# Kernel tuning notes

Measured on AMD Instinct MI355X. Metric: run time of the kernel, lower is better.

Reference implementation:

```python
import jax, jax.numpy as jnp
import numpy as np

N = 100000
K = 16
E = N * K
IN_DIM = 16
MLP_DIMS = (32, 32, 16)


def setup_inputs() -> dict:
    key = jax.random.key(0)
    ks = jax.random.split(key, 10)
    feats = jax.random.normal(ks[0], (N, IN_DIM), dtype=jnp.float32)
    xyz = jax.random.normal(ks[1], (N, 3), dtype=jnp.float32)
    neighbors_index = jax.random.randint(ks[2], (E,), 0, N, dtype=jnp.int32)
    neighbors_row_splits = (jnp.arange(N + 1, dtype=jnp.int32) * K)
    neighbors_distance = jax.random.uniform(ks[3], (E,), dtype=jnp.float32)
    # MLP params: 4 -> 32 (relu) -> 32 (relu) -> IN_DIM * MLP_DIMS[-1]
    def dense(k, fan_in, fan_out):
        lim = np.sqrt(6.0 / (fan_in + fan_out)).astype(np.float32)
        W = jax.random.uniform(k, (fan_in, fan_out), minval=-lim, maxval=lim, dtype=jnp.float32)
        b = jnp.zeros((fan_out,), dtype=jnp.float32)
        return W, b
    W1, b1 = dense(ks[4], 4, MLP_DIMS[0])
    W2, b2 = dense(ks[5], MLP_DIMS[0], MLP_DIMS[1])
    W3, b3 = dense(ks[6], MLP_DIMS[1], IN_DIM * MLP_DIMS[2])
    return {"feats": feats, "xyz": xyz, "neighbors_index": neighbors_index,
            "neighbors_row_splits": neighbors_row_splits,
            "neighbors_distance": neighbors_distance,
            "W1": W1, "b1": b1, "W2": W2, "b2": b2, "W3": W3, "b3": b3}


def reference(feats, xyz, neighbors_index, neighbors_row_splits, neighbors_distance,
              W1, b1, W2, b2, W3, b3):
    n_queries = neighbors_row_splits.shape[0] - 1
    counts = neighbors_row_splits[1:] - neighbors_row_splits[:-1]
    # ragged row_splits -> per-edge segment ids (query index per edge)
    segment_ids = jnp.repeat(jnp.arange(n_queries, dtype=jnp.int32), counts,
                             total_repeat_length=neighbors_index.shape[0])
    # gather neighbor coords, subtract query coords
    diff = xyz[neighbors_index] - xyz[segment_ids]          # [E, 3]
    d = jax.lax.stop_gradient(neighbors_distance)
    r = jnp.sqrt(d + 1e-7)                                   # [E]
    polar = jnp.stack([r, diff[:, 0] / r, diff[:, 2] / r, diff[:, 1] / r], axis=-1)  # [E, 4]
    # per-edge MLP producing dynamic weight matrices
    h = jax.nn.relu(polar @ W1 + b1)
    h = jax.nn.relu(h @ W2 + b2)
    w = (h @ W3 + b3).reshape(-1, IN_DIM, MLP_DIMS[2])       # [E, in_dim, out]
    neighbor_feats = feats[neighbors_index]                  # [E, in_dim]
    edge_out = jnp.einsum('ei,eio->eo', neighbor_feats, w)   # [E, out]
    new_feats = jax.ops.segment_sum(edge_out, segment_ids, num_segments=n_queries)
    return new_feats
```

## Files before the change

### kernel.cpp

```cpp
#include <hip/hip_runtime.h>


constexpr int THREADS = 256;
constexpr int NBLOCKS = 1024;

typedef __attribute__((ext_vector_type(8)))  short short8;
typedef __attribute__((ext_vector_type(4)))  int   intx4;
typedef __attribute__((ext_vector_type(16))) float floatx16;
typedef __attribute__((ext_vector_type(2)))  float floatx2;

static __device__ inline short f2bf(float x) {
  __bf16 b = (__bf16)x;
  return __builtin_bit_cast(short, b);
}
static __device__ inline unsigned pk2(float lo, float hi) {
  unsigned l = (unsigned short)__builtin_bit_cast(unsigned short, f2bf(lo));
  unsigned h = (unsigned short)__builtin_bit_cast(unsigned short, f2bf(hi));
  return (h << 16) | l;
}

template <int CTRL>
static __device__ inline float dpp_add(float x) {
  int y = __builtin_amdgcn_update_dpp(0, __builtin_bit_cast(int, x),
                                      CTRL, 0xF, 0xF, true);
  return x + __builtin_bit_cast(float, y);
}

__global__ __launch_bounds__(THREADS, 2) void polarconv_v14(
    const float* __restrict__ feats,
    const float* __restrict__ xyz,
    const int*   __restrict__ nbr,
    const float* __restrict__ dist,
    const float* __restrict__ W1,
    const float* __restrict__ b1,
    const float* __restrict__ W2,
    const float* __restrict__ b2,
    const float* __restrict__ W3,
    const float* __restrict__ b3,
    float* __restrict__ out,
    int Nq)
{
  const int tid  = threadIdx.x;
  const int lane = tid & 63;
  const int col  = lane & 31;
  const int g2   = lane >> 5;
  const int qh   = col >> 4;
  const int c16  = col & 15;
  const int E    = Nq * 16;

  __shared__ alignas(16) short sBU[1024 * 8];
  short8* sBU8 = reinterpret_cast<short8*>(sBU);
  for (int s = tid; s < 1024; s += THREADS) {
    const int t2h = s >> 6, ln = s & 63;
    const int t2 = t2h >> 1, h = t2h & 1;
    const int cc = ln & 31, gg = ln >> 5;
    short8 v;
#pragma unroll
    for (int j = 0; j < 8; ++j)
      v[j] = f2bf(W3[(16 * h + (j & 3) + 8 * (j >> 2) + 4 * gg) * 256 + t2 * 32 + cc]);
    sBU8[s] = v;
  }
  __syncthreads();
  const short8* buP = sBU8 + lane;

  short8 a1;
#pragma unroll
  for (int j = 0; j < 8; ++j) {
    short v = 0;
    if (g2 == 0) {
      if (j < 4)       v = f2bf(W1[j * 32 + col]);
      else if (j == 4) v = f2bf(b1[col]);
    }
    a1[j] = v;
  }
  short8 a2k[2];
#pragma unroll
  for (int h = 0; h < 2; ++h)
#pragma unroll
    for (int j = 0; j < 8; ++j)
      a2k[h][j] = f2bf(W2[(16 * h + (j & 3) + 8 * (j >> 2) + 4 * g2) * 32 + col]);
  short8 ab3;
#pragma unroll
  for (int j = 0; j < 8; ++j)
    ab3[j] = (col < 16) ? f2bf(b3[(8 * g2 + j) * 16 + col]) : (short)0;

  floatx16 z16;
#pragma unroll
  for (int m = 0; m < 16; ++m) z16[m] = 0.0f;

  const int wid   = blockIdx.x * (THREADS / 64) + (tid >> 6);
  const int STR   = NBLOCKS * (THREADS / 64);
  const int pairs = (Nq + 1) >> 1;
  int p = wid;
  if (p >= pairs) return;

  int   nbN;
  float dN, cxN, cyN, czN, nxN, nyN, nzN;
  {
    const int e = min(p * 32 + col, E - 1);
    nbN = nbr[e];
    dN  = dist[e];
    const int qc = min(2 * p + qh, Nq - 1);
    cxN = xyz[3 * qc]; cyN = xyz[3 * qc + 1]; czN = xyz[3 * qc + 2];
    nxN = xyz[3 * nbN]; nyN = xyz[3 * nbN + 1]; nzN = xyz[3 * nbN + 2];
  }

  for (; p < pairs; p += STR) {
    const int   nbA = nbN;
    const float dA = dN, cx = cxN, cy = cyN, cz = czN;
    const float nx = nxN, ny = nyN, nz = nzN;

    const float4* fp = reinterpret_cast<const float4*>(feats + (size_t)nbA * 16);
    float4 v0 = fp[0], v1 = fp[1], v2 = fp[2], v3 = fp[3];

    const int pc = min(p + STR, pairs - 1);
    {
      const int e2 = min(pc * 32 + col, E - 1);
      nbN = nbr[e2];
      dN  = dist[e2];
      const int qc2 = min(2 * pc + qh, Nq - 1);
      cxN = xyz[3 * qc2]; cyN = xyz[3 * qc2 + 1]; czN = xyz[3 * qc2 + 2];
    }

    const float rr  = sqrtf(dA + 1e-7f);
    const float inv = 1.0f / rr;
    const float q0 = rr;
    const float q1 = (nx - cx) * inv;
    const float q2 = (nz - cz) * inv;
    const float q3 = (ny - cy) * inv;

    short8 bp;
    bp[0] = (g2 == 0) ? f2bf(q0) : (short)0;
    bp[1] = (g2 == 0) ? f2bf(q1) : (short)0;
    bp[2] = (g2 == 0) ? f2bf(q2) : (short)0;
    bp[3] = (g2 == 0) ? f2bf(q3) : (short)0;
    bp[4] = (g2 == 0) ? (short)0x3F80 : (short)0;
    bp[5] = 0; bp[6] = 0; bp[7] = 0;

    floatx16 d1 = __builtin_amdgcn_mfma_f32_32x32x16_bf16(a1, bp, z16, 0, 0, 0);
    short8 bh1k0, bh1k1;
#pragma unroll
    for (int j = 0; j < 8; ++j) {
      bh1k0[j] = f2bf(fmaxf(d1[j], 0.0f));
      bh1k1[j] = f2bf(fmaxf(d1[8 + j], 0.0f));
    }

    floatx16 t0 = __builtin_amdgcn_mfma_f32_32x32x16_bf16(a2k[0], bh1k0, z16, 0, 0, 0);
    floatx16 d2 = __builtin_amdgcn_mfma_f32_32x32x16_bf16(a2k[1], bh1k1, t0, 0, 0, 0);
    short8 bh2k0, bh2k1;
#pragma unroll
    for (int j = 0; j < 8; ++j) {
      const int c0 = (j & 3) + 8 * (j >> 2);
      const float bl0 = g2 ? b2[c0 + 4]      : b2[c0];
      const float bl1 = g2 ? b2[16 + c0 + 4] : b2[16 + c0];
      bh2k0[j] = f2bf(fmaxf(d2[j]     + bl0, 0.0f));
      bh2k1[j] = f2bf(fmaxf(d2[8 + j] + bl1, 0.0f));
    }

    nxN = xyz[3 * nbN]; nyN = xyz[3 * nbN + 1]; nzN = xyz[3 * nbN + 2];

    unsigned fpk0 = pk2(v0.x, v0.y), fpk1 = pk2(v0.z, v0.w);
    unsigned fpk2 = pk2(v1.x, v1.y), fpk3 = pk2(v1.z, v1.w);
    unsigned fpk4 = pk2(v2.x, v2.y), fpk5 = pk2(v2.z, v2.w);
    unsigned fpk6 = pk2(v3.x, v3.y), fpk7 = pk2(v3.z, v3.w);

    intx4 bsel;
    bsel[0] = (int)(g2 ? fpk4 : fpk0);
    bsel[1] = (int)(g2 ? fpk5 : fpk1);
    bsel[2] = (int)(g2 ? fpk6 : fpk2);
    bsel[3] = (int)(g2 ? fpk7 : fpk3);
    short8 bf3 = __builtin_bit_cast(short8, bsel);
    floatx16 s3 = __builtin_amdgcn_mfma_f32_32x32x16_bf16(ab3, bf3, z16, 0, 0, 0);
    floatx2 Sb[4];
#pragma unroll
    for (int r = 0; r < 4; ++r) { Sb[r][0] = s3[2 * r]; Sb[r][1] = s3[2 * r + 1]; }

#pragma unroll
    for (int t2 = 0; t2 < 8; ++t2) {
      short8 w0 = buP[(t2 * 2 + 0) * 64];
      short8 w1 = buP[(t2 * 2 + 1) * 64];
      floatx16 u0 = __builtin_amdgcn_mfma_f32_32x32x16_bf16(w0, bh2k0, z16, 0, 0, 0);
      floatx16 dd = __builtin_amdgcn_mfma_f32_32x32x16_bf16(w1, bh2k1, u0, 0, 0, 0);
      unsigned fw;
      switch (t2) {
        case 0: fw = fpk0; break; case 1: fw = fpk1; break;
        case 2: fw = fpk2; break; case 3: fw = fpk3; break;
        case 4: fw = fpk4; break; case 5: fw = fpk5; break;
        case 6: fw = fpk6; break; default: fw = fpk7; break;
      }
      const float fe = __builtin_bit_cast(float, (int)(fw << 16));
      const float fo = __builtin_bit_cast(float, (int)(fw & 0xffff0000u));
      const floatx2 fe2 = {fe, fe}, fo2 = {fo, fo};
#pragma unroll
      for (int r = 0; r < 4; ++r) {
        floatx2 lo = {dd[2 * r],     dd[2 * r + 1]};
        floatx2 hi = {dd[8 + 2 * r], dd[8 + 2 * r + 1]};
        Sb[r] = __builtin_elementwise_fma(fe2, lo, Sb[r]);
        Sb[r] = __builtin_elementwise_fma(fo2, hi, Sb[r]);
      }
      if (t2 & 1) __builtin_amdgcn_sched_barrier(0);
    }

    float Sa[8];
#pragma unroll
    for (int r = 0; r < 4; ++r) { Sa[2 * r] = Sb[r][0]; Sa[2 * r + 1] = Sb[r][1]; }

#pragma unroll
    for (int j = 0; j < 8; ++j) Sa[j] = dpp_add<0xB1>(Sa[j]);
#pragma unroll
    for (int j = 0; j < 8; ++j) Sa[j] = dpp_add<0x4E>(Sa[j]);
#pragma unroll
    for (int j = 0; j < 8; ++j) Sa[j] = dpp_add<0x124>(Sa[j]);
#pragma unroll
    for (int j = 0; j < 8; ++j) Sa[j] = dpp_add<0x128>(Sa[j]);

    if (c16 == 0) {
      const int qq = 2 * p + qh;
      if (qq < Nq) {
        float* op = out + (size_t)qq * 16 + 4 * g2;
        float4 lo = {Sa[0], Sa[1], Sa[2], Sa[3]};
        float4 hi = {Sa[4], Sa[5], Sa[6], Sa[7]};
        *reinterpret_cast<float4*>(op)     = lo;
        *reinterpret_cast<float4*>(op + 8) = hi;
      }
    }
  }
}

extern "C" void kernel_launch(void* const* d_in, const int* in_sizes, int n_in,
                              void* d_out, int out_size, void* d_ws, size_t ws_size,
                              hipStream_t stream) {
  const float* feats = (const float*)d_in[0];
  const float* xyz   = (const float*)d_in[1];
  const int*   nbr   = (const int*)d_in[2];
  const float* dist  = (const float*)d_in[4];
  const float* W1 = (const float*)d_in[5];
  const float* b1 = (const float*)d_in[6];
  const float* W2 = (const float*)d_in[7];
  const float* b2 = (const float*)d_in[8];
  const float* W3 = (const float*)d_in[9];
  const float* b3 = (const float*)d_in[10];
  float* out = (float*)d_out;

  const int Nq = in_sizes[3] - 1;

  polarconv_v14<<<NBLOCKS, THREADS, 0, stream>>>(
      feats, xyz, nbr, dist, W1, b1, W2, b2, W3, b3, out, Nq);
}
```

Before: 56.99 us.

## Software-pipeline MLP layers 1-2 of next pair with layer-3 contraction of current pair

Splits the per-pair work into two phases: phase1 computes the first two MLP layers and packs the features, and phase2 runs the W3 MFMA contraction, the reduction and the store. The loop now runs phase1 for the next pair before phase2 for the current one, with index and coordinate loads prefetched two iterations ahead. The aim is to overlap the dependent MFMA chains and memory latency of two pairs. The sched_barrier hints are removed, and carrying a second set of live state raises register pressure, which may cut occupancy or cause spills.

```diff
diff --git a/kernel.cpp b/kernel.cpp
--- a/kernel.cpp
+++ b/kernel.cpp
@@ -26,7 +26,12 @@
   return x + __builtin_bit_cast(float, y);
 }
 
-__global__ __launch_bounds__(THREADS, 2) void polarconv_v14(
+struct P1out {
+  short8 bh0, bh1;
+  unsigned f[8];
+};
+
+__global__ __launch_bounds__(THREADS, 2) void polarconv_v16(
     const float* __restrict__ feats,
     const float* __restrict__ xyz,
     const int*   __restrict__ nbr,
@@ -88,41 +93,11 @@
 #pragma unroll
   for (int m = 0; m < 16; ++m) z16[m] = 0.0f;
 
-  const int wid   = blockIdx.x * (THREADS / 64) + (tid >> 6);
-  const int STR   = NBLOCKS * (THREADS / 64);
-  const int pairs = (Nq + 1) >> 1;
-  int p = wid;
-  if (p >= pairs) return;
-
-  int   nbN;
-  float dN, cxN, cyN, czN, nxN, nyN, nzN;
-  {
-    const int e = min(p * 32 + col, E - 1);
-    nbN = nbr[e];
-    dN  = dist[e];
-    const int qc = min(2 * p + qh, Nq - 1);
-    cxN = xyz[3 * qc]; cyN = xyz[3 * qc + 1]; czN = xyz[3 * qc + 2];
-    nxN = xyz[3 * nbN]; nyN = xyz[3 * nbN + 1]; nzN = xyz[3 * nbN + 2];
-  }
-
-  for (; p < pairs; p += STR) {
-    const int   nbA = nbN;
-    const float dA = dN, cx = cxN, cy = cyN, cz = czN;
-    const float nx = nxN, ny = nyN, nz = nzN;
-
-    const float4* fp = reinterpret_cast<const float4*>(feats + (size_t)nbA * 16);
-    float4 v0 = fp[0], v1 = fp[1], v2 = fp[2], v3 = fp[3];
-
-    const int pc = min(p + STR, pairs - 1);
-    {
-      const int e2 = min(pc * 32 + col, E - 1);
-      nbN = nbr[e2];
-      dN  = dist[e2];
-      const int qc2 = min(2 * pc + qh, Nq - 1);
-      cxN = xyz[3 * qc2]; cyN = xyz[3 * qc2 + 1]; czN = xyz[3 * qc2 + 2];
-    }
-
-    const float rr  = sqrtf(dA + 1e-7f);
+  auto phase1 = [&](float dd, float cx, float cy, float cz,
+                    float nx, float ny, float nz,
+                    float4 v0, float4 v1, float4 v2, float4 v3) -> P1out {
+    P1out o;
+    const float rr  = sqrtf(dd + 1e-7f);
     const float inv = 1.0f / rr;
     const float q0 = rr;
     const float q1 = (nx - cx) * inv;
@@ -144,31 +119,29 @@
       bh1k0[j] = f2bf(fmaxf(d1[j], 0.0f));
       bh1k1[j] = f2bf(fmaxf(d1[8 + j], 0.0f));
     }
-
     floatx16 t0 = __builtin_amdgcn_mfma_f32_32x32x16_bf16(a2k[0], bh1k0, z16, 0, 0, 0);
     floatx16 d2 = __builtin_amdgcn_mfma_f32_32x32x16_bf16(a2k[1], bh1k1, t0, 0, 0, 0);
-    short8 bh2k0, bh2k1;
 #pragma unroll
     for (int j = 0; j < 8; ++j) {
       const int c0 = (j & 3) + 8 * (j >> 2);
       const float bl0 = g2 ? b2[c0 + 4]      : b2[c0];
       const float bl1 = g2 ? b2[16 + c0 + 4] : b2[16 + c0];
-      bh2k0[j] = f2bf(fmaxf(d2[j]     + bl0, 0.0f));
-      bh2k1[j] = f2bf(fmaxf(d2[8 + j] + bl1, 0.0f));
-    }
-
-    nxN = xyz[3 * nbN]; nyN = xyz[3 * nbN + 1]; nzN = xyz[3 * nbN + 2];
-
-    unsigned fpk0 = pk2(v0.x, v0.y), fpk1 = pk2(v0.z, v0.w);
-    unsigned fpk2 = pk2(v1.x, v1.y), fpk3 = pk2(v1.z, v1.w);
-    unsigned fpk4 = pk2(v2.x, v2.y), fpk5 = pk2(v2.z, v2.w);
-    unsigned fpk6 = pk2(v3.x, v3.y), fpk7 = pk2(v3.z, v3.w);
-
+      o.bh0[j] = f2bf(fmaxf(d2[j]     + bl0, 0.0f));
+      o.bh1[j] = f2bf(fmaxf(d2[8 + j] + bl1, 0.0f));
+    }
+    o.f[0] = pk2(v0.x, v0.y); o.f[1] = pk2(v0.z, v0.w);
+    o.f[2] = pk2(v1.x, v1.y); o.f[3] = pk2(v1.z, v1.w);
+    o.f[4] = pk2(v2.x, v2.y); o.f[5] = pk2(v2.z, v2.w);
+    o.f[6] = pk2(v3.x, v3.y); o.f[7] = pk2(v3.z, v3.w);
+    return o;
+  };
+
+  auto phase2 = [&](const P1out& s, int pq) {
     intx4 bsel;
-    bsel[0] = (int)(g2 ? fpk4 : fpk0);
-    bsel[1] = (int)(g2 ? fpk5 : fpk1);
-    bsel[2] = (int)(g2 ? fpk6 : fpk2);
-    bsel[3] = (int)(g2 ? fpk7 : fpk3);
+    bsel[0] = (int)(g2 ? s.f[4] : s.f[0]);
+    bsel[1] = (int)(g2 ? s.f[5] : s.f[1]);
+    bsel[2] = (int)(g2 ? s.f[6] : s.f[2]);
+    bsel[3] = (int)(g2 ? s.f[7] : s.f[3]);
     short8 bf3 = __builtin_bit_cast(short8, bsel);
     floatx16 s3 = __builtin_amdgcn_mfma_f32_32x32x16_bf16(ab3, bf3, z16, 0, 0, 0);
     floatx2 Sb[4];
@@ -179,15 +152,9 @@
     for (int t2 = 0; t2 < 8; ++t2) {
       short8 w0 = buP[(t2 * 2 + 0) * 64];
       short8 w1 = buP[(t2 * 2 + 1) * 64];
-      floatx16 u0 = __builtin_amdgcn_mfma_f32_32x32x16_bf16(w0, bh2k0, z16, 0, 0, 0);
-      floatx16 dd = __builtin_amdgcn_mfma_f32_32x32x16_bf16(w1, bh2k1, u0, 0, 0, 0);
-      unsigned fw;
-      switch (t2) {
-        case 0: fw = fpk0; break; case 1: fw = fpk1; break;
-        case 2: fw = fpk2; break; case 3: fw = fpk3; break;
-        case 4: fw = fpk4; break; case 5: fw = fpk5; break;
-        case 6: fw = fpk6; break; default: fw = fpk7; break;
-      }
+      floatx16 u0 = __builtin_amdgcn_mfma_f32_32x32x16_bf16(w0, s.bh0, z16, 0, 0, 0);
+      floatx16 dd = __builtin_amdgcn_mfma_f32_32x32x16_bf16(w1, s.bh1, u0, 0, 0, 0);
+      const unsigned fw = s.f[t2];
       const float fe = __builtin_bit_cast(float, (int)(fw << 16));
       const float fo = __builtin_bit_cast(float, (int)(fw & 0xffff0000u));
       const floatx2 fe2 = {fe, fe}, fo2 = {fo, fo};
@@ -198,13 +165,11 @@
         Sb[r] = __builtin_elementwise_fma(fe2, lo, Sb[r]);
         Sb[r] = __builtin_elementwise_fma(fo2, hi, Sb[r]);
       }
-      if (t2 & 1) __builtin_amdgcn_sched_barrier(0);
     }
 
     float Sa[8];
 #pragma unroll
     for (int r = 0; r < 4; ++r) { Sa[2 * r] = Sb[r][0]; Sa[2 * r + 1] = Sb[r][1]; }
-
 #pragma unroll
     for (int j = 0; j < 8; ++j) Sa[j] = dpp_add<0xB1>(Sa[j]);
 #pragma unroll
@@ -215,7 +180,7 @@
     for (int j = 0; j < 8; ++j) Sa[j] = dpp_add<0x128>(Sa[j]);
 
     if (c16 == 0) {
-      const int qq = 2 * p + qh;
+      const int qq = 2 * pq + qh;
       if (qq < Nq) {
         float* op = out + (size_t)qq * 16 + 4 * g2;
         float4 lo = {Sa[0], Sa[1], Sa[2], Sa[3]};
@@ -224,6 +189,60 @@
         *reinterpret_cast<float4*>(op + 8) = hi;
       }
     }
+  };
+
+  const int wid   = blockIdx.x * (THREADS / 64) + (tid >> 6);
+  const int STR   = NBLOCKS * (THREADS / 64);
+  const int pairs = (Nq + 1) >> 1;
+  int pA = wid;
+  if (pA >= pairs) return;
+
+  P1out SA;
+  int   nbN;
+  float dN, cxN, cyN, czN, nxN, nyN, nzN;
+  {
+    const int e0 = min(pA * 32 + col, E - 1);
+    const int nb0 = nbr[e0];
+    const float d0 = dist[e0];
+    const int qc0 = min(2 * pA + qh, Nq - 1);
+    const float cx0 = xyz[3 * qc0], cy0 = xyz[3 * qc0 + 1], cz0 = xyz[3 * qc0 + 2];
+    const float nx0 = xyz[3 * nb0], ny0 = xyz[3 * nb0 + 1], nz0 = xyz[3 * nb0 + 2];
+    const float4* fp = reinterpret_cast<const float4*>(feats + (size_t)nb0 * 16);
+    SA = phase1(d0, cx0, cy0, cz0, nx0, ny0, nz0, fp[0], fp[1], fp[2], fp[3]);
+
+    const int pB0 = min(pA + STR, pairs - 1);
+    const int eB  = min(pB0 * 32 + col, E - 1);
+    nbN = nbr[eB];
+    dN  = dist[eB];
+    const int qb = min(2 * pB0 + qh, Nq - 1);
+    cxN = xyz[3 * qb]; cyN = xyz[3 * qb + 1]; czN = xyz[3 * qb + 2];
+    nxN = xyz[3 * nbN]; nyN = xyz[3 * nbN + 1]; nzN = xyz[3 * nbN + 2];
+  }
+
+  for (;;) {
+    const float4* fp = reinterpret_cast<const float4*>(feats + (size_t)nbN * 16);
+    float4 v0 = fp[0], v1 = fp[1], v2 = fp[2], v3 = fp[3];
+
+    const int pB = min(pA + STR, pairs - 1);
+    const int pC = min(pB + STR, pairs - 1);
+    const int eC = min(pC * 32 + col, E - 1);
+    const int nbC = nbr[eC];
+    const float dC = dist[eC];
+    const int qcC = min(2 * pC + qh, Nq - 1);
+    const float cxC = xyz[3 * qcC], cyC = xyz[3 * qcC + 1], czC = xyz[3 * qcC + 2];
+
+    P1out SB = phase1(dN, cxN, cyN, czN, nxN, nyN, nzN, v0, v1, v2, v3);
+
+    const float nxC = xyz[3 * nbC], nyC = xyz[3 * nbC + 1], nzC = xyz[3 * nbC + 2];
+
+    phase2(SA, pA);
+
+    SA = SB;
+    nbN = nbC; dN = dC;
+    cxN = cxC; cyN = cyC; czN = czC;
+    nxN = nxC; nyN = nyC; nzN = nzC;
+    pA += STR;
+    if (pA >= pairs) break;
   }
 }
 
@@ -244,6 +263,6 @@
 
   const int Nq = in_sizes[3] - 1;
 
-  polarconv_v14<<<NBLOCKS, THREADS, 0, stream>>>(
+  polarconv_v16<<<NBLOCKS, THREADS, 0, stream>>>(
       feats, xyz, nbr, dist, W1, b1, W2, b2, W3, b3, out, Nq);
 }
```

New measurement: 62.54 us. 1.1x slower.
